# Kernel optimization log

Hardware: AMD Instinct MI355X
Metric: run time of the kernel (lower is better)

## Reference

```python
import jax, jax.numpy as jnp
import numpy as np
import math

B, S, D_MODEL, H, CLIP = 4, 1024, 1024, 16, 16
HEAD_DIM = D_MODEL // H
NEG = -1e6


def setup_inputs() -> dict:
    key = jax.random.key(0)
    ks = jax.random.split(key, 10)
    scale = 1.0 / math.sqrt(D_MODEL)
    return {
        "queries": jax.random.normal(ks[0], (B, S, D_MODEL), jnp.float32),
        "keys": jax.random.normal(ks[1], (B, S, D_MODEL), jnp.float32),
        "values": jax.random.normal(ks[2], (B, S, D_MODEL), jnp.float32),
        "valid_lens": jax.random.randint(ks[3], (B,), 1, S + 1),
        "Wq": jax.random.normal(ks[4], (D_MODEL, D_MODEL), jnp.float32) * scale,
        "Wk": jax.random.normal(ks[5], (D_MODEL, D_MODEL), jnp.float32) * scale,
        "Wv": jax.random.normal(ks[6], (D_MODEL, D_MODEL), jnp.float32) * scale,
        "Wo": jax.random.normal(ks[7], (D_MODEL, D_MODEL), jnp.float32) * scale,
        "Ek": jax.random.normal(ks[8], (2 * CLIP + 1, HEAD_DIM), jnp.float32),
        "Ev": jax.random.normal(ks[9], (2 * CLIP + 1, HEAD_DIM), jnp.float32),
    }


def _split_heads(x):
    # [B, S, D] -> [B*H, S, head_dim]
    b, s, _ = x.shape
    return x.reshape(b, s, H, HEAD_DIM).transpose(0, 2, 1, 3).reshape(b * H, s, HEAD_DIM)


def reference(queries, keys, values, valid_lens, Wq, Wk, Wv, Wo, Ek, Ev):
    q = _split_heads(queries @ Wq.T)  # [BH, S, d]
    k = _split_heads(keys @ Wk.T)
    v = _split_heads(values @ Wv.T)

    # relative-position tables, shared across batch and heads: [Sq, Sk, d]
    rng = jnp.arange(S)
    dist = jnp.clip(rng[None, :] - rng[:, None], -CLIP, CLIP) + CLIP
    pos_k = Ek[dist]
    pos_v = Ev[dist]

    scores = jnp.einsum('bqd,bkd->bqk', q, k) + jnp.einsum('bqd,qkd->bqk', q, pos_k)
    scores = scores / math.sqrt(HEAD_DIM)

    vl = jnp.repeat(valid_lens, H)  # [B*H]
    mask = jnp.arange(S)[None, None, :] < vl[:, None, None]
    attn = jax.nn.softmax(jnp.where(mask, scores, NEG), axis=-1)

    out = jnp.einsum('bqk,bkd->bqd', attn, v) + jnp.einsum('bqk,qkd->bqd', attn, pos_v)

    # merge heads: [B*H, S, d] -> [B, S, D]
    out = out.reshape(B, H, S, HEAD_DIM).transpose(0, 2, 1, 3).reshape(B, S, D_MODEL)
    return out @ Wo.T
```

## Files before the change

### kernel.cpp

```cpp
#include <hip/hip_runtime.h>


typedef __attribute__((ext_vector_type(8))) short short8;
typedef __attribute__((ext_vector_type(4))) float floatx4;

__device__ __forceinline__ unsigned short f2bf(float f) {
  union { float f; unsigned u; } v; v.f = f;
  return (unsigned short)((v.u + 0x7fffu + ((v.u >> 16) & 1u)) >> 16);
}
__device__ __forceinline__ unsigned packbf(float lo, float hi) {
  return ((unsigned)f2bf(hi) << 16) | (unsigned)f2bf(lo);
}

__device__ __forceinline__ void gld16(const void* g, void* l) {
  __builtin_amdgcn_global_load_lds(
      (const __attribute__((address_space(1))) unsigned*)g,
      (__attribute__((address_space(3))) unsigned*)l, 16, 0, 0);
}

#define WS_XQ  ((size_t)0)
#define WS_XK  ((size_t)4194304)
#define WS_XV  ((size_t)8388608)
#define WS_W   ((size_t)12582912)
#define WS_EKB ((size_t)16777216)
#define WS_EVT ((size_t)16781312)
#define WS_QB  ((size_t)16785408)
#define WS_KB  ((size_t)20979712)
#define WS_VT  ((size_t)25174016)
#define WS_OB  ((size_t)0)

__global__ __launch_bounds__(256) void convert_all_kernel(
    const float* __restrict__ q, const float* __restrict__ k,
    const float* __restrict__ v,
    const float* __restrict__ wq, const float* __restrict__ wk,
    const float* __restrict__ wv, const float* __restrict__ wo,
    const float* __restrict__ Ek, const float* __restrict__ Ev,
    const int* __restrict__ valid_lens, unsigned short* __restrict__ ws) {
  int z = blockIdx.z;
  if (z < 3) {
    const float* src = z == 0 ? q : (z == 1 ? k : v);
    unsigned short* dst = ws + (size_t)z * 4194304;
    size_t i = ((size_t)blockIdx.x * 256 + threadIdx.x) * 8;
    if (z > 0) {
      int b = (int)(i >> 20), s = (int)((i >> 10) & 1023);
      if (s >= valid_lens[b]) return;
    }
    float4 a = *(const float4*)(src + i);
    float4 bb = *(const float4*)(src + i + 4);
    uint4 o = { packbf(a.x, a.y), packbf(a.z, a.w), packbf(bb.x, bb.y), packbf(bb.z, bb.w) };
    *(uint4*)(dst + i) = o;
  } else if (z < 7) {
    if (blockIdx.x >= 512) return;
    const float* src = (z == 3) ? wq : (z == 4 ? wk : (z == 5 ? wv : wo));
    unsigned short* dst = ws + WS_W + (size_t)(z - 3) * 1048576;
    size_t i = ((size_t)blockIdx.x * 256 + threadIdx.x) * 8;
    float4 a = *(const float4*)(src + i);
    float4 bb = *(const float4*)(src + i + 4);
    uint4 o = { packbf(a.x, a.y), packbf(a.z, a.w), packbf(bb.x, bb.y), packbf(bb.z, bb.w) };
    *(uint4*)(dst + i) = o;
  } else {
    if (blockIdx.x >= 4) return;
    int gid = blockIdx.x * 256 + threadIdx.x;
    unsigned short* ekb = ws + WS_EKB;
    int i0 = gid * 8;
    unsigned short vals[8];
#pragma unroll
    for (int u = 0; u < 8; u++) {
      int i = i0 + u;
      if (i < 4096) {
        int t = i >> 6, d = i & 63;
        vals[u] = (t < 33) ? f2bf(Ek[t * 64 + d]) : (unsigned short)0;
      } else {
        int j = i - 4096;
        int d = j >> 6, t = j & 63;
        vals[u] = (t < 33) ? f2bf(Ev[t * 64 + d]) : (unsigned short)0;
      }
    }
    *(uint4*)(ekb + i0) = *(uint4*)vals;
  }
}

__device__ __forceinline__ void gemm128_body(
    const unsigned short* __restrict__ A, const unsigned short* __restrict__ W,
    unsigned short* __restrict__ Cb, float* __restrict__ Cf, int mode, float scale) {
  __shared__ unsigned short sA[128 * 32];
  __shared__ unsigned short sB[128 * 32];
  const int tid = threadIdx.x, wave = tid >> 6, lane = tid & 63;
  const int lr = lane & 15, lq = lane >> 4;
  const int wr = wave >> 1, wc = wave & 1;
  const int m0 = blockIdx.y * 128, n0 = blockIdx.x * 128;
  const int srow = lane >> 2, scol = (lane & 3) * 8;

  const unsigned short* gA0 = A + (size_t)(m0 + wave * 16 + srow) * 1024 + scol;
  const unsigned short* gA1 = gA0 + (size_t)64 * 1024;
  const unsigned short* gB0 = W + (size_t)(n0 + wave * 16 + srow) * 1024 + scol;
  const unsigned short* gB1 = gB0 + (size_t)64 * 1024;
  unsigned short* lA0 = sA + wave * 512;  unsigned short* lA1 = lA0 + 2048;
  unsigned short* lB0 = sB + wave * 512;  unsigned short* lB1 = lB0 + 2048;

  floatx4 acc[4][4];
#pragma unroll
  for (int mi = 0; mi < 4; mi++)
#pragma unroll
    for (int ni = 0; ni < 4; ni++) acc[mi][ni] = (floatx4){0.f, 0.f, 0.f, 0.f};

  for (int k0 = 0; k0 < 1024; k0 += 32) {
    gld16(gA0 + k0, lA0); gld16(gA1 + k0, lA1);
    gld16(gB0 + k0, lB0); gld16(gB1 + k0, lB1);
    __syncthreads();
    short8 af[4], bf[4];
#pragma unroll
    for (int mi = 0; mi < 4; mi++)
      af[mi] = *(const short8*)(sA + (wr * 64 + mi * 16 + lr) * 32 + lq * 8);
#pragma unroll
    for (int ni = 0; ni < 4; ni++)
      bf[ni] = *(const short8*)(sB + (wc * 64 + ni * 16 + lr) * 32 + lq * 8);
#pragma unroll
    for (int mi = 0; mi < 4; mi++)
#pragma unroll
      for (int ni = 0; ni < 4; ni++)
        acc[mi][ni] = __builtin_amdgcn_mfma_f32_16x16x32_bf16(af[mi], bf[ni], acc[mi][ni], 0, 0, 0);
    __syncthreads();
  }

  if (mode == 2) {
#pragma unroll
    for (int mi = 0; mi < 4; mi++)
#pragma unroll
      for (int ni = 0; ni < 4; ni++) {
        int col = n0 + wc * 64 + ni * 16 + lr;
        int h = col >> 6, d = col & 63;
        int rowg = m0 + wr * 64 + mi * 16 + lq * 4;
        int b = rowg >> 10, s = rowg & 1023;
        uint2 pk;
        pk.x = packbf(acc[mi][ni][0], acc[mi][ni][1]);
        pk.y = packbf(acc[mi][ni][2], acc[mi][ni][3]);
        *(uint2*)(Cb + ((size_t)((b * 16 + h) * 64 + d) << 10) + s) = pk;
      }
  } else if (mode == 3) {
#pragma unroll
    for (int mi = 0; mi < 4; mi++)
#pragma unroll
      for (int ni = 0; ni < 4; ni++)
#pragma unroll
        for (int r = 0; r < 4; r++) {
          int row = m0 + wr * 64 + mi * 16 + lq * 4 + r;
          int col = n0 + wc * 64 + ni * 16 + lr;
          Cf[(size_t)row * 1024 + col] = acc[mi][ni][r];
        }
  } else {
#pragma unroll
    for (int mi = 0; mi < 4; mi++)
#pragma unroll
      for (int ni = 0; ni < 4; ni++)
#pragma unroll
        for (int r = 0; r < 4; r++) {
          int row = m0 + wr * 64 + mi * 16 + lq * 4 + r;
          int col = n0 + wc * 64 + ni * 16 + lr;
          Cb[(size_t)row * 1024 + col] = f2bf(acc[mi][ni][r] * scale);
        }
  }
}

__global__ __launch_bounds__(256, 3) void proj_qkv_kernel(
    unsigned short* __restrict__ ws, const int* __restrict__ valid_lens) {
  int z = blockIdx.z;
  if (z > 0) {
    int m0 = blockIdx.y * 128;
    if ((m0 & 1023) >= valid_lens[m0 >> 10]) return;
  }
  const unsigned short* A = ws + (size_t)z * 4194304;
  const unsigned short* W = ws + WS_W + (size_t)z * 1048576;
  unsigned short* Cb = (z == 0) ? ws + WS_QB : (z == 1 ? ws + WS_KB : ws + WS_VT);
  int mode = (z == 2) ? 2 : (z == 0 ? 0 : 1);
  float scale = (z == 0) ? 0.125f : 1.0f;
  gemm128_body(A, W, Cb, nullptr, mode, scale);
}

__global__ __launch_bounds__(256, 3) void out_proj_kernel(
    const unsigned short* __restrict__ Ob, const unsigned short* __restrict__ Wo,
    float* __restrict__ out) {
  gemm128_body(Ob, Wo, nullptr, out, 3, 1.f);
}

__global__ __launch_bounds__(64, 2) void attn_rpr_kernel(
    const unsigned short* __restrict__ Qb, const unsigned short* __restrict__ Kb,
    const unsigned short* __restrict__ Vt, const int* __restrict__ valid_lens,
    const unsigned short* __restrict__ Ekb, const unsigned short* __restrict__ Evtb,
    unsigned short* __restrict__ Ob) {
  __shared__ unsigned short sP[32 * 72];
  __shared__ float sQE[32 * 34];
  __shared__ float sW[32 * 34];

  const int lane = threadIdx.x;
  const int lr = lane & 15, lq = lane >> 4;
  const int bh = blockIdx.x, qx = blockIdx.y;
  const int b = bh >> 4;
  const int vlen = valid_lens[b];
  const int i0 = qx * 32;
  const int colh = (bh & 15) * 64;
  const size_t bat = (size_t)b * 1024 * 1024;
  const int rbase = lq * 4;

  for (int i = lane; i < 32 * 34; i += 64) sW[i] = 0.f;

  const unsigned short* gQ = Qb + bat + (size_t)(i0 + lr) * 1024 + colh + lq * 8;
  short8 aq0[2], aq1[2];
#pragma unroll
  for (int g = 0; g < 2; g++) {
    aq0[g] = *(const short8*)(gQ + (size_t)g * 16 * 1024);
    aq1[g] = *(const short8*)(gQ + (size_t)g * 16 * 1024 + 32);
  }

#pragma unroll
  for (int ni = 0; ni < 3; ni++) {
    short8 be0 = *(const short8*)(Ekb + (ni * 16 + lr) * 64 + lq * 8);
    short8 be1 = *(const short8*)(Ekb + (ni * 16 + lr) * 64 + 32 + lq * 8);
    int t = ni * 16 + lr;
#pragma unroll
    for (int g = 0; g < 2; g++) {
      floatx4 aqe = (floatx4){0.f, 0.f, 0.f, 0.f};
      aqe = __builtin_amdgcn_mfma_f32_16x16x32_bf16(aq0[g], be0, aqe, 0, 0, 0);
      aqe = __builtin_amdgcn_mfma_f32_16x16x32_bf16(aq1[g], be1, aqe, 0, 0, 0);
      if (t < 33)
#pragma unroll
        for (int r = 0; r < 4; r++) sQE[(g * 16 + rbase + r) * 34 + t] = aqe[r];
    }
  }

  floatx4 acc_o[2][4];
#pragma unroll
  for (int g = 0; g < 2; g++)
#pragma unroll
    for (int nd = 0; nd < 4; nd++) acc_o[g][nd] = (floatx4){0.f, 0.f, 0.f, 0.f};
  float rs0[2][4] = {{0.f,0.f,0.f,0.f},{0.f,0.f,0.f,0.f}};
  float rs32[2][4] = {{0.f,0.f,0.f,0.f},{0.f,0.f,0.f,0.f}};

  const int vcl = vlen < 1024 ? vlen : 1024;
  const int kt_max = (vcl + 63) >> 6;

  const unsigned short* gK = Kb + bat + colh;
  const unsigned short* gV = Vt + ((size_t)bh * 64) * 1024;

  for (int kt = 0; kt < kt_max; kt++) {
    const int j0 = kt * 64;

    short8 bk[4][2];
#pragma unroll
    for (int ni = 0; ni < 4; ni++) {
      const unsigned short* p = gK + (size_t)(j0 + ni * 16 + lr) * 1024 + lq * 8;
      bk[ni][0] = *(const short8*)(p);
      bk[ni][1] = *(const short8*)(p + 32);
    }

    floatx4 accs[2][4];
    __builtin_amdgcn_s_setprio(1);
#pragma unroll
    for (int g = 0; g < 2; g++)
#pragma unroll
      for (int ni = 0; ni < 4; ni++) {
        accs[g][ni] = (floatx4){0.f, 0.f, 0.f, 0.f};
        accs[g][ni] = __builtin_amdgcn_mfma_f32_16x16x32_bf16(aq0[g], bk[ni][0], accs[g][ni], 0, 0, 0);
        accs[g][ni] = __builtin_amdgcn_mfma_f32_16x16x32_bf16(aq1[g], bk[ni][1], accs[g][ni], 0, 0, 0);
      }
    __builtin_amdgcn_s_setprio(0);

    short8 bv[4][2];
#pragma unroll
    for (int nd = 0; nd < 4; nd++) {
      const unsigned short* p = gV + (size_t)(nd * 16 + lr) * 1024 + j0 + lq * 8;
      bv[nd][0] = *(const short8*)(p);
      bv[nd][1] = *(const short8*)(p + 32);
    }

    const bool general = (j0 > i0 - 79) && (j0 < i0 + 47);
    if (!general) {
      const bool hi = (j0 >= i0 + 47);
      const int tconst = hi ? 32 : 0;
#pragma unroll
      for (int g = 0; g < 2; g++) {
        float qe[4];
#pragma unroll
        for (int r = 0; r < 4; r++) qe[r] = sQE[(g * 16 + rbase + r) * 34 + tconst];
#pragma unroll
        for (int ni = 0; ni < 4; ni++)
#pragma unroll
          for (int r = 0; r < 4; r++) {
            int j_g = j0 + ni * 16 + lr;
            float pv = (j_g < vlen) ? __expf(accs[g][ni][r] + qe[r]) : 0.f;
            if (hi) rs32[g][r] += pv; else rs0[g][r] += pv;
            sP[(g * 16 + rbase + r) * 72 + ni * 16 + lr] = f2bf(pv);
          }
      }
    } else {
#pragma unroll
      for (int g = 0; g < 2; g++)
#pragma unroll
        for (int ni = 0; ni < 4; ni++)
#pragma unroll
          for (int r = 0; r < 4; r++) {
            int i_g = i0 + g * 16 + rbase + r;
            int j_g = j0 + ni * 16 + lr;
            int dd = j_g - i_g; dd = dd < -16 ? -16 : (dd > 16 ? 16 : dd);
            int t = dd + 16;
            float pv = (j_g < vlen) ? __expf(accs[g][ni][r] + sQE[(g * 16 + rbase + r) * 34 + t]) : 0.f;
            atomicAdd(&sW[(g * 16 + rbase + r) * 34 + t], pv);
            sP[(g * 16 + rbase + r) * 72 + ni * 16 + lr] = f2bf(pv);
          }
    }

    __builtin_amdgcn_s_setprio(1);
#pragma unroll
    for (int g = 0; g < 2; g++) {
      short8 ap0 = *(const short8*)(sP + (g * 16 + lr) * 72 + lq * 8);
      short8 ap1 = *(const short8*)(sP + (g * 16 + lr) * 72 + 32 + lq * 8);
#pragma unroll
      for (int nd = 0; nd < 4; nd++) {
        acc_o[g][nd] = __builtin_amdgcn_mfma_f32_16x16x32_bf16(ap0, bv[nd][0], acc_o[g][nd], 0, 0, 0);
        acc_o[g][nd] = __builtin_amdgcn_mfma_f32_16x16x32_bf16(ap1, bv[nd][1], acc_o[g][nd], 0, 0, 0);
      }
    }
    __builtin_amdgcn_s_setprio(0);
  }

#pragma unroll
  for (int x = 1; x < 16; x <<= 1)
#pragma unroll
    for (int g = 0; g < 2; g++)
#pragma unroll
      for (int r = 0; r < 4; r++) {
        rs0[g][r] += __shfl_xor(rs0[g][r], x, 64);
        rs32[g][r] += __shfl_xor(rs32[g][r], x, 64);
      }
  if (lr == 0)
#pragma unroll
    for (int g = 0; g < 2; g++)
#pragma unroll
      for (int r = 0; r < 4; r++) {
        sW[(g * 16 + rbase + r) * 34 + 0] += rs0[g][r];
        sW[(g * 16 + rbase + r) * 34 + 32] += rs32[g][r];
      }

  {
    int row = lane >> 2;
    int c0 = (lane & 3) * 16;
    unsigned* sP32 = (unsigned*)sP;
#pragma unroll
    for (int g = 0; g < 2; g++)
#pragma unroll
      for (int q = 0; q < 8; q++) {
        int t0 = c0 + 2 * q, t1 = t0 + 1;
        float w0 = (t0 < 33) ? sW[(g * 16 + row) * 34 + t0] : 0.f;
        float w1 = (t1 < 33) ? sW[(g * 16 + row) * 34 + t1] : 0.f;
        sP32[(g * 16 + row) * 36 + (c0 >> 1) + q] = packbf(w0, w1);
      }
  }
#pragma unroll
  for (int g = 0; g < 2; g++) {
    short8 aw0 = *(const short8*)(sP + (g * 16 + lr) * 72 + lq * 8);
    short8 aw1 = *(const short8*)(sP + (g * 16 + lr) * 72 + 32 + lq * 8);
#pragma unroll
    for (int nd = 0; nd < 4; nd++) {
      short8 be0 = *(const short8*)(Evtb + (nd * 16 + lr) * 64 + lq * 8);
      short8 be1 = *(const short8*)(Evtb + (nd * 16 + lr) * 64 + 32 + lq * 8);
      acc_o[g][nd] = __builtin_amdgcn_mfma_f32_16x16x32_bf16(aw0, be0, acc_o[g][nd], 0, 0, 0);
      acc_o[g][nd] = __builtin_amdgcn_mfma_f32_16x16x32_bf16(aw1, be1, acc_o[g][nd], 0, 0, 0);
    }
  }

#pragma unroll
  for (int g = 0; g < 2; g++) {
    float linv[4];
#pragma unroll
    for (int r = 0; r < 4; r++) {
      float l = 0.f;
#pragma unroll
      for (int t = 0; t < 33; t++) l += sW[(g * 16 + rbase + r) * 34 + t];
      linv[r] = 1.f / l;
    }
#pragma unroll
    for (int nd = 0; nd < 4; nd++)
#pragma unroll
      for (int r = 0; r < 4; r++) {
        int row = i0 + g * 16 + rbase + r;
        Ob[bat + (size_t)row * 1024 + colh + nd * 16 + lr] =
            f2bf(acc_o[g][nd][r] * linv[r]);
      }
  }
}

extern "C" void kernel_launch(void* const* d_in, const int* in_sizes, int n_in,
                              void* d_out, int out_size, void* d_ws, size_t ws_size,
                              hipStream_t stream) {
  const float* queries = (const float*)d_in[0];
  const float* keys    = (const float*)d_in[1];
  const float* values  = (const float*)d_in[2];
  const int* valid_lens = (const int*)d_in[3];
  const float* Wq = (const float*)d_in[4];
  const float* Wk = (const float*)d_in[5];
  const float* Wv = (const float*)d_in[6];
  const float* Wo = (const float*)d_in[7];
  const float* Ek = (const float*)d_in[8];
  const float* Ev = (const float*)d_in[9];
  float* out = (float*)d_out;
  unsigned short* ws = (unsigned short*)d_ws;

  convert_all_kernel<<<dim3(2048, 1, 8), 256, 0, stream>>>(
      queries, keys, values, Wq, Wk, Wv, Wo, Ek, Ev, valid_lens, ws);
  proj_qkv_kernel<<<dim3(8, 32, 3), 256, 0, stream>>>(ws, valid_lens);
  attn_rpr_kernel<<<dim3(64, 32), 64, 0, stream>>>(
      ws + WS_QB, ws + WS_KB, ws + WS_VT, valid_lens, ws + WS_EKB, ws + WS_EVT, ws + WS_OB);
  out_proj_kernel<<<dim3(8, 32), 256, 0, stream>>>(ws + WS_OB, ws + WS_W + 3145728, out);
}
```

Baseline: 225.7 us.

## Process 64 query rows per attention block to reuse K/V tile loads

Each single-wave attention block now handles 64 query rows instead of 32, running two 32-row passes over every loaded K/V tile. This halves the number of blocks and the global K/V loads per query row, cutting memory traffic. In exchange it raises register pressure (more Q fragments and output accumulators) and LDS use, and leaves fewer blocks (1024), which may hurt occupancy and load balance on the GPU.

```diff
diff --git a/kernel.cpp b/kernel.cpp
--- a/kernel.cpp
+++ b/kernel.cpp
@@ -188,26 +188,26 @@
     const unsigned short* __restrict__ Vt, const int* __restrict__ valid_lens,
     const unsigned short* __restrict__ Ekb, const unsigned short* __restrict__ Evtb,
     unsigned short* __restrict__ Ob) {
-  __shared__ unsigned short sP[32 * 72];
-  __shared__ float sQE[32 * 34];
-  __shared__ float sW[32 * 34];
+  __shared__ unsigned short sP[64 * 72];
+  __shared__ float sQE[64 * 34];
+  __shared__ float sW[64 * 34];
 
   const int lane = threadIdx.x;
   const int lr = lane & 15, lq = lane >> 4;
   const int bh = blockIdx.x, qx = blockIdx.y;
   const int b = bh >> 4;
   const int vlen = valid_lens[b];
-  const int i0 = qx * 32;
+  const int i0 = qx * 64;
   const int colh = (bh & 15) * 64;
   const size_t bat = (size_t)b * 1024 * 1024;
   const int rbase = lq * 4;
 
-  for (int i = lane; i < 32 * 34; i += 64) sW[i] = 0.f;
+  for (int i = lane; i < 64 * 34; i += 64) sW[i] = 0.f;
 
   const unsigned short* gQ = Qb + bat + (size_t)(i0 + lr) * 1024 + colh + lq * 8;
-  short8 aq0[2], aq1[2];
-#pragma unroll
-  for (int g = 0; g < 2; g++) {
+  short8 aq0[4], aq1[4];
+#pragma unroll
+  for (int g = 0; g < 4; g++) {
     aq0[g] = *(const short8*)(gQ + (size_t)g * 16 * 1024);
     aq1[g] = *(const short8*)(gQ + (size_t)g * 16 * 1024 + 32);
   }
@@ -218,7 +218,7 @@
     short8 be1 = *(const short8*)(Ekb + (ni * 16 + lr) * 64 + 32 + lq * 8);
     int t = ni * 16 + lr;
 #pragma unroll
-    for (int g = 0; g < 2; g++) {
+    for (int g = 0; g < 4; g++) {
       floatx4 aqe = (floatx4){0.f, 0.f, 0.f, 0.f};
       aqe = __builtin_amdgcn_mfma_f32_16x16x32_bf16(aq0[g], be0, aqe, 0, 0, 0);
       aqe = __builtin_amdgcn_mfma_f32_16x16x32_bf16(aq1[g], be1, aqe, 0, 0, 0);
@@ -228,13 +228,17 @@
     }
   }
 
-  floatx4 acc_o[2][4];
-#pragma unroll
-  for (int g = 0; g < 2; g++)
+  floatx4 acc_o[4][4];
+#pragma unroll
+  for (int g = 0; g < 4; g++)
 #pragma unroll
     for (int nd = 0; nd < 4; nd++) acc_o[g][nd] = (floatx4){0.f, 0.f, 0.f, 0.f};
-  float rs0[2][4] = {{0.f,0.f,0.f,0.f},{0.f,0.f,0.f,0.f}};
-  float rs32[2][4] = {{0.f,0.f,0.f,0.f},{0.f,0.f,0.f,0.f}};
+  float rs0[4][4];
+  float rs32[4][4];
+#pragma unroll
+  for (int g = 0; g < 4; g++)
+#pragma unroll
+    for (int r = 0; r < 4; r++) { rs0[g][r] = 0.f; rs32[g][r] = 0.f; }
 
   const int vcl = vlen < 1024 ? vlen : 1024;
   const int kt_max = (vcl + 63) >> 6;
@@ -252,19 +256,6 @@
       bk[ni][0] = *(const short8*)(p);
       bk[ni][1] = *(const short8*)(p + 32);
     }
-
-    floatx4 accs[2][4];
-    __builtin_amdgcn_s_setprio(1);
-#pragma unroll
-    for (int g = 0; g < 2; g++)
-#pragma unroll
-      for (int ni = 0; ni < 4; ni++) {
-        accs[g][ni] = (floatx4){0.f, 0.f, 0.f, 0.f};
-        accs[g][ni] = __builtin_amdgcn_mfma_f32_16x16x32_bf16(aq0[g], bk[ni][0], accs[g][ni], 0, 0, 0);
-        accs[g][ni] = __builtin_amdgcn_mfma_f32_16x16x32_bf16(aq1[g], bk[ni][1], accs[g][ni], 0, 0, 0);
-      }
-    __builtin_amdgcn_s_setprio(0);
-
     short8 bv[4][2];
 #pragma unroll
     for (int nd = 0; nd < 4; nd++) {
@@ -273,60 +264,82 @@
       bv[nd][1] = *(const short8*)(p + 32);
     }
 
-    const bool general = (j0 > i0 - 79) && (j0 < i0 + 47);
-    if (!general) {
-      const bool hi = (j0 >= i0 + 47);
-      const int tconst = hi ? 32 : 0;
-#pragma unroll
-      for (int g = 0; g < 2; g++) {
-        float qe[4];
-#pragma unroll
-        for (int r = 0; r < 4; r++) qe[r] = sQE[(g * 16 + rbase + r) * 34 + tconst];
-#pragma unroll
-        for (int ni = 0; ni < 4; ni++)
-#pragma unroll
-          for (int r = 0; r < 4; r++) {
-            int j_g = j0 + ni * 16 + lr;
-            float pv = (j_g < vlen) ? __expf(accs[g][ni][r] + qe[r]) : 0.f;
-            if (hi) rs32[g][r] += pv; else rs0[g][r] += pv;
-            sP[(g * 16 + rbase + r) * 72 + ni * 16 + lr] = f2bf(pv);
-          }
-      }
-    } else {
-#pragma unroll
-      for (int g = 0; g < 2; g++)
-#pragma unroll
-        for (int ni = 0; ni < 4; ni++)
-#pragma unroll
-          for (int r = 0; r < 4; r++) {
-            int i_g = i0 + g * 16 + rbase + r;
-            int j_g = j0 + ni * 16 + lr;
-            int dd = j_g - i_g; dd = dd < -16 ? -16 : (dd > 16 ? 16 : dd);
-            int t = dd + 16;
-            float pv = (j_g < vlen) ? __expf(accs[g][ni][r] + sQE[(g * 16 + rbase + r) * 34 + t]) : 0.f;
-            atomicAdd(&sW[(g * 16 + rbase + r) * 34 + t], pv);
-            sP[(g * 16 + rbase + r) * 72 + ni * 16 + lr] = f2bf(pv);
-          }
-    }
-
-    __builtin_amdgcn_s_setprio(1);
-#pragma unroll
-    for (int g = 0; g < 2; g++) {
-      short8 ap0 = *(const short8*)(sP + (g * 16 + lr) * 72 + lq * 8);
-      short8 ap1 = *(const short8*)(sP + (g * 16 + lr) * 72 + 32 + lq * 8);
-#pragma unroll
-      for (int nd = 0; nd < 4; nd++) {
-        acc_o[g][nd] = __builtin_amdgcn_mfma_f32_16x16x32_bf16(ap0, bv[nd][0], acc_o[g][nd], 0, 0, 0);
-        acc_o[g][nd] = __builtin_amdgcn_mfma_f32_16x16x32_bf16(ap1, bv[nd][1], acc_o[g][nd], 0, 0, 0);
-      }
-    }
-    __builtin_amdgcn_s_setprio(0);
+#pragma unroll
+    for (int p = 0; p < 2; p++) {
+      const int g0 = 2 * p;
+      const int ip0 = i0 + 32 * p;
+
+      floatx4 accs[2][4];
+      __builtin_amdgcn_s_setprio(1);
+#pragma unroll
+      for (int gg = 0; gg < 2; gg++)
+#pragma unroll
+        for (int ni = 0; ni < 4; ni++) {
+          accs[gg][ni] = (floatx4){0.f, 0.f, 0.f, 0.f};
+          accs[gg][ni] = __builtin_amdgcn_mfma_f32_16x16x32_bf16(aq0[g0 + gg], bk[ni][0], accs[gg][ni], 0, 0, 0);
+          accs[gg][ni] = __builtin_amdgcn_mfma_f32_16x16x32_bf16(aq1[g0 + gg], bk[ni][1], accs[gg][ni], 0, 0, 0);
+        }
+      __builtin_amdgcn_s_setprio(0);
+
+      const bool general = (j0 > ip0 - 79) && (j0 < ip0 + 47);
+      if (!general) {
+        const bool hi = (j0 >= ip0 + 47);
+        const int tconst = hi ? 32 : 0;
+#pragma unroll
+        for (int gg = 0; gg < 2; gg++) {
+          const int g = g0 + gg;
+          float qe[4];
+#pragma unroll
+          for (int r = 0; r < 4; r++) qe[r] = sQE[(g * 16 + rbase + r) * 34 + tconst];
+#pragma unroll
+          for (int ni = 0; ni < 4; ni++)
+#pragma unroll
+            for (int r = 0; r < 4; r++) {
+              int j_g = j0 + ni * 16 + lr;
+              float pv = (j_g < vlen) ? __expf(accs[gg][ni][r] + qe[r]) : 0.f;
+              if (hi) rs32[g][r] += pv; else rs0[g][r] += pv;
+              sP[(g * 16 + rbase + r) * 72 + ni * 16 + lr] = f2bf(pv);
+            }
+        }
+      } else {
+#pragma unroll
+        for (int gg = 0; gg < 2; gg++) {
+          const int g = g0 + gg;
+#pragma unroll
+          for (int ni = 0; ni < 4; ni++)
+#pragma unroll
+            for (int r = 0; r < 4; r++) {
+              int i_g = i0 + g * 16 + rbase + r;
+              int j_g = j0 + ni * 16 + lr;
+              int dd = j_g - i_g; dd = dd < -16 ? -16 : (dd > 16 ? 16 : dd);
+              int t = dd + 16;
+              float pv = (j_g < vlen) ? __expf(accs[gg][ni][r] + sQE[(g * 16 + rbase + r) * 34 + t]) : 0.f;
+              atomicAdd(&sW[(g * 16 + rbase + r) * 34 + t], pv);
+              sP[(g * 16 + rbase + r) * 72 + ni * 16 + lr] = f2bf(pv);
+            }
+        }
+      }
+
+      __builtin_amdgcn_s_setprio(1);
+#pragma unroll
+      for (int gg = 0; gg < 2; gg++) {
+        const int g = g0 + gg;
+        short8 ap0 = *(const short8*)(sP + (g * 16 + lr) * 72 + lq * 8);
+        short8 ap1 = *(const short8*)(sP + (g * 16 + lr) * 72 + 32 + lq * 8);
+#pragma unroll
+        for (int nd = 0; nd < 4; nd++) {
+          acc_o[g][nd] = __builtin_amdgcn_mfma_f32_16x16x32_bf16(ap0, bv[nd][0], acc_o[g][nd], 0, 0, 0);
+          acc_o[g][nd] = __builtin_amdgcn_mfma_f32_16x16x32_bf16(ap1, bv[nd][1], acc_o[g][nd], 0, 0, 0);
+        }
+      }
+      __builtin_amdgcn_s_setprio(0);
+    }
   }
 
 #pragma unroll
   for (int x = 1; x < 16; x <<= 1)
 #pragma unroll
-    for (int g = 0; g < 2; g++)
+    for (int g = 0; g < 4; g++)
 #pragma unroll
       for (int r = 0; r < 4; r++) {
         rs0[g][r] += __shfl_xor(rs0[g][r], x, 64);
@@ -334,7 +347,7 @@
       }
   if (lr == 0)
 #pragma unroll
-    for (int g = 0; g < 2; g++)
+    for (int g = 0; g < 4; g++)
 #pragma unroll
       for (int r = 0; r < 4; r++) {
         sW[(g * 16 + rbase + r) * 34 + 0] += rs0[g][r];
@@ -346,7 +359,7 @@
     int c0 = (lane & 3) * 16;
     unsigned* sP32 = (unsigned*)sP;
 #pragma unroll
-    for (int g = 0; g < 2; g++)
+    for (int g = 0; g < 4; g++)
 #pragma unroll
       for (int q = 0; q < 8; q++) {
         int t0 = c0 + 2 * q, t1 = t0 + 1;
@@ -356,7 +369,7 @@
       }
   }
 #pragma unroll
-  for (int g = 0; g < 2; g++) {
+  for (int g = 0; g < 4; g++) {
     short8 aw0 = *(const short8*)(sP + (g * 16 + lr) * 72 + lq * 8);
     short8 aw1 = *(const short8*)(sP + (g * 16 + lr) * 72 + 32 + lq * 8);
 #pragma unroll
@@ -369,7 +382,7 @@
   }
 
 #pragma unroll
-  for (int g = 0; g < 2; g++) {
+  for (int g = 0; g < 4; g++) {
     float linv[4];
 #pragma unroll
     for (int r = 0; r < 4; r++) {
@@ -408,7 +421,7 @@
   convert_all_kernel<<<dim3(2048, 1, 8), 256, 0, stream>>>(
       queries, keys, values, Wq, Wk, Wv, Wo, Ek, Ev, valid_lens, ws);
   proj_qkv_kernel<<<dim3(8, 32, 3), 256, 0, stream>>>(ws, valid_lens);
-  attn_rpr_kernel<<<dim3(64, 32), 64, 0, stream>>>(
+  attn_rpr_kernel<<<dim3(64, 16), 64, 0, stream>>>(
       ws + WS_QB, ws + WS_KB, ws + WS_VT, valid_lens, ws + WS_EKB, ws + WS_EVT, ws + WS_OB);
   out_proj_kernel<<<dim3(8, 32), 256, 0, stream>>>(ws + WS_OB, ws + WS_W + 3145728, out);
 }
```

Result: slower. 256.1 us (+13.5%).

## Store K and V in MFMA-fragment tiled layout for contiguous attention loads

Applied to the files above, without the earlier changes.

The projection epilogues now write K and V into a per-head, fragment-ordered layout so that each lane in the attention kernel reads one contiguous 1 KB block per MFMA operand, instead of strided rows 2 KB apart. V loads are also hoisted next to K loads, so both are in flight before the QK MFMAs. The cost is that the K epilogue now does scattered scalar bf16 stores, and holding more registers live at once may cut occupancy.

```diff
diff --git a/kernel.cpp b/kernel.cpp
--- a/kernel.cpp
+++ b/kernel.cpp
@@ -132,11 +132,32 @@
         int h = col >> 6, d = col & 63;
         int rowg = m0 + wr * 64 + mi * 16 + lq * 4;
         int b = rowg >> 10, s = rowg & 1023;
+        int bh = b * 16 + h;
         uint2 pk;
         pk.x = packbf(acc[mi][ni][0], acc[mi][ni][1]);
         pk.y = packbf(acc[mi][ni][2], acc[mi][ni][3]);
-        *(uint2*)(Cb + ((size_t)((b * 16 + h) * 64 + d) << 10) + s) = pk;
-      }
+        size_t off = (size_t)bh * 65536
+                   + (size_t)((s >> 6) * 8 + (d >> 4) * 2 + ((s >> 5) & 1)) * 512
+                   + (size_t)((((s >> 3) & 3) * 16) + (d & 15)) * 8 + (s & 7);
+        *(uint2*)(Cb + off) = pk;
+      }
+  } else if (mode == 1) {
+#pragma unroll
+    for (int mi = 0; mi < 4; mi++)
+#pragma unroll
+      for (int ni = 0; ni < 4; ni++)
+#pragma unroll
+        for (int r = 0; r < 4; r++) {
+          int rowg = m0 + wr * 64 + mi * 16 + lq * 4 + r;
+          int col = n0 + wc * 64 + ni * 16 + lr;
+          int b = rowg >> 10, s = rowg & 1023;
+          int h = col >> 6, d = col & 63;
+          int bh = b * 16 + h;
+          size_t off = (size_t)bh * 65536
+                     + (size_t)((s >> 6) * 8 + ((s & 63) >> 4) * 2 + (d >> 5)) * 512
+                     + (size_t)((((d & 31) >> 3) * 16) + (s & 15)) * 8 + (d & 7);
+          Cb[off] = f2bf(acc[mi][ni][r]);
+        }
   } else if (mode == 3) {
 #pragma unroll
     for (int mi = 0; mi < 4; mi++)
@@ -184,8 +205,8 @@
 }
 
 __global__ __launch_bounds__(64, 2) void attn_rpr_kernel(
-    const unsigned short* __restrict__ Qb, const unsigned short* __restrict__ Kb,
-    const unsigned short* __restrict__ Vt, const int* __restrict__ valid_lens,
+    const unsigned short* __restrict__ Qb, const unsigned short* __restrict__ Kf,
+    const unsigned short* __restrict__ Vf, const int* __restrict__ valid_lens,
     const unsigned short* __restrict__ Ekb, const unsigned short* __restrict__ Evtb,
     unsigned short* __restrict__ Ob) {
   __shared__ unsigned short sP[32 * 72];
@@ -239,18 +260,22 @@
   const int vcl = vlen < 1024 ? vlen : 1024;
   const int kt_max = (vcl + 63) >> 6;
 
-  const unsigned short* gK = Kb + bat + colh;
-  const unsigned short* gV = Vt + ((size_t)bh * 64) * 1024;
+  const unsigned short* gKf = Kf + (size_t)bh * 65536 + lane * 8;
+  const unsigned short* gVf = Vf + (size_t)bh * 65536 + lane * 8;
 
   for (int kt = 0; kt < kt_max; kt++) {
     const int j0 = kt * 64;
 
-    short8 bk[4][2];
+    short8 bk[4][2], bv[4][2];
 #pragma unroll
     for (int ni = 0; ni < 4; ni++) {
-      const unsigned short* p = gK + (size_t)(j0 + ni * 16 + lr) * 1024 + lq * 8;
-      bk[ni][0] = *(const short8*)(p);
-      bk[ni][1] = *(const short8*)(p + 32);
+      bk[ni][0] = *(const short8*)(gKf + (size_t)(kt * 8 + ni * 2 + 0) * 512);
+      bk[ni][1] = *(const short8*)(gKf + (size_t)(kt * 8 + ni * 2 + 1) * 512);
+    }
+#pragma unroll
+    for (int nd = 0; nd < 4; nd++) {
+      bv[nd][0] = *(const short8*)(gVf + (size_t)(kt * 8 + nd * 2 + 0) * 512);
+      bv[nd][1] = *(const short8*)(gVf + (size_t)(kt * 8 + nd * 2 + 1) * 512);
     }
 
     floatx4 accs[2][4];
@@ -264,14 +289,6 @@
         accs[g][ni] = __builtin_amdgcn_mfma_f32_16x16x32_bf16(aq1[g], bk[ni][1], accs[g][ni], 0, 0, 0);
       }
     __builtin_amdgcn_s_setprio(0);
-
-    short8 bv[4][2];
-#pragma unroll
-    for (int nd = 0; nd < 4; nd++) {
-      const unsigned short* p = gV + (size_t)(nd * 16 + lr) * 1024 + j0 + lq * 8;
-      bv[nd][0] = *(const short8*)(p);
-      bv[nd][1] = *(const short8*)(p + 32);
-    }
 
     const bool general = (j0 > i0 - 79) && (j0 < i0 + 47);
     if (!general) {
```

New measurement: 222.5 us. No clear change (-1.4%).
